# Performance work log

Hardware: AMD Instinct MI355X
Metric: run time of the kernel (lower is better)

## Reference

```python
import jax, jax.numpy as jnp
import numpy as np
from jax import lax

DN = ('NCHW', 'OIHW', 'NCHW')


def _dwconv(x, w, pad_h, pad_w):
    # depthwise conv: feature_group_count == channels
    C = x.shape[1]
    return lax.conv_general_dilated(
        x, w, window_strides=(1, 1),
        padding=[(pad_h, pad_h), (pad_w, pad_w)],
        dimension_numbers=DN, feature_group_count=C)


def setup_inputs() -> dict:
    key = jax.random.key(0)
    ks = jax.random.split(key, 6)
    B, C, H, W = 8, 64, 256, 256
    K = 21
    x = jax.random.normal(ks[0], (B, C, H, W), dtype=jnp.float32)
    local_w = jax.random.normal(ks[1], (C, 1, 5, 5), dtype=jnp.float32) * (2.0 / 25) ** 0.5
    h_w = jax.random.normal(ks[2], (C, 1, 1, K), dtype=jnp.float32) * (2.0 / K) ** 0.5
    v_w = jax.random.normal(ks[3], (C, 1, K, 1), dtype=jnp.float32) * (2.0 / K) ** 0.5
    pw_w = jax.random.normal(ks[4], (C, C, 1, 1), dtype=jnp.float32) * (1.0 / C) ** 0.5
    gamma = jnp.ones((C,), dtype=jnp.float32)
    beta = jnp.zeros((C,), dtype=jnp.float32)
    mean = jnp.zeros((C,), dtype=jnp.float32)
    var = jnp.ones((C,), dtype=jnp.float32)
    return {"x": x, "local_w": local_w, "h_w": h_w, "v_w": v_w,
            "pw_w": pw_w, "gamma": gamma, "beta": beta, "mean": mean, "var": var}


def reference(x, local_w, h_w, v_w, pw_w, gamma, beta, mean, var):
    eps = 1e-5
    attn = _dwconv(x, local_w, 2, 2)        # 5x5 depthwise
    attn = _dwconv(attn, h_w, 0, 10)        # 1x21 depthwise
    attn = _dwconv(attn, v_w, 10, 0)        # 21x1 depthwise
    attn = lax.conv_general_dilated(        # 1x1 pointwise (full mix)
        attn, pw_w, (1, 1), [(0, 0), (0, 0)], dimension_numbers=DN)
    # BatchNorm (inference mode with running stats) fused with sigmoid gate
    inv = gamma * lax.rsqrt(var + eps)
    attn = attn * inv[None, :, None, None] + (beta - mean * inv)[None, :, None, None]
    return x * jax.nn.sigmoid(attn)
```

## Files before the change

kernel.cpp:

```cpp
#include <hip/hip_runtime.h>
#include <hip/hip_bf16.h>

#define BB 8
#define CC 64
#define HH 256
#define WW 256

__device__ __forceinline__ unsigned short f2bf(float f) {
    __hip_bfloat16 h = __float2bfloat16(f);
    return *reinterpret_cast<unsigned short*>(&h);
}
__device__ __forceinline__ float bf2f(unsigned short u) {
    unsigned int v = ((unsigned int)u) << 16;
    float r;
    __builtin_memcpy(&r, &v, 4);
    return r;
}
__device__ __forceinline__ float bflo(unsigned int u) {
    unsigned int v = u << 16;
    float r; __builtin_memcpy(&r, &v, 4); return r;
}
__device__ __forceinline__ float bfhi(unsigned int u) {
    unsigned int v = u & 0xffff0000u;
    float r; __builtin_memcpy(&r, &v, 4); return r;
}

__global__ __launch_bounds__(512) void k1_local_h(
        const float* __restrict__ x, const float* __restrict__ lw,
        const float* __restrict__ hw, unsigned short* __restrict__ a2out) {
    const int strip = blockIdx.x;
    const int bc    = blockIdx.y;
    const int c     = bc & (CC - 1);
    const int y0    = strip * 32;
    const int tid   = threadIdx.x;

    __shared__ float4 xs4[36][66];
    __shared__ float4 a1_4[32][70];

    const float* xbase = x + (size_t)bc * (HH * WW);

    if (tid < 192) {
        int rr = tid / 6, g = tid % 6;
        a1_4[rr][g < 3 ? g : 64 + g] = make_float4(0.f, 0.f, 0.f, 0.f);
    }
    for (int i = tid; i < 36 * 66; i += 512) {
        int rr = i / 66, g = i - rr * 66;
        int gy = y0 - 2 + rr;
        float4 v = make_float4(0.f, 0.f, 0.f, 0.f);
        if (gy >= 0 && gy < HH && g >= 1 && g <= 64)
            v = *reinterpret_cast<const float4*>(xbase + (size_t)gy * WW + 4 * (g - 1));
        xs4[rr][g] = v;
    }
    __syncthreads();

    const int cg = tid & 31;
    const int rp = tid >> 5;
    const float* lwc = lw + c * 25;

    float acc0[8], acc1[8];
    #pragma unroll
    for (int j = 0; j < 8; ++j) { acc0[j] = 0.f; acc1[j] = 0.f; }

    #pragma unroll
    for (int t = 0; t < 6; ++t) {
        float4 g0 = xs4[2 * rp + t][2 * cg + 0];
        float4 g1 = xs4[2 * rp + t][2 * cg + 1];
        float4 g2 = xs4[2 * rp + t][2 * cg + 2];
        float4 g3 = xs4[2 * rp + t][2 * cg + 3];
        float f[16] = {g0.x, g0.y, g0.z, g0.w, g1.x, g1.y, g1.z, g1.w,
                       g2.x, g2.y, g2.z, g2.w, g3.x, g3.y, g3.z, g3.w};
        if (t < 5) {
            #pragma unroll
            for (int kx = 0; kx < 5; ++kx) {
                float wv = lwc[t * 5 + kx];
                #pragma unroll
                for (int j = 0; j < 8; ++j)
                    acc0[j] = fmaf(wv, f[j + kx + 2], acc0[j]);
            }
        }
        if (t >= 1) {
            #pragma unroll
            for (int kx = 0; kx < 5; ++kx) {
                float wv = lwc[(t - 1) * 5 + kx];
                #pragma unroll
                for (int j = 0; j < 8; ++j)
                    acc1[j] = fmaf(wv, f[j + kx + 2], acc1[j]);
            }
        }
    }
    a1_4[2 * rp + 0][2 * cg + 3] = make_float4(acc0[0], acc0[1], acc0[2], acc0[3]);
    a1_4[2 * rp + 0][2 * cg + 4] = make_float4(acc0[4], acc0[5], acc0[6], acc0[7]);
    a1_4[2 * rp + 1][2 * cg + 3] = make_float4(acc1[0], acc1[1], acc1[2], acc1[3]);
    a1_4[2 * rp + 1][2 * cg + 4] = make_float4(acc1[4], acc1[5], acc1[6], acc1[7]);
    __syncthreads();

    const float* hwc = hw + c * 21;
    #pragma unroll
    for (int row = 0; row < 2; ++row) {
        float fw[32];
        #pragma unroll
        for (int t2 = 0; t2 < 8; ++t2) {
            float4 g = a1_4[2 * rp + row][2 * cg + t2];
            fw[4 * t2 + 0] = g.x; fw[4 * t2 + 1] = g.y;
            fw[4 * t2 + 2] = g.z; fw[4 * t2 + 3] = g.w;
        }
        float o[8];
        #pragma unroll
        for (int j = 0; j < 8; ++j) o[j] = 0.f;
        #pragma unroll
        for (int k = 0; k < 21; ++k) {
            float wv = hwc[k];
            #pragma unroll
            for (int j = 0; j < 8; ++j)
                o[j] = fmaf(wv, fw[j + k + 2], o[j]);
        }
        unsigned short* dst = a2out + (size_t)(bc * HH + y0 + 2 * rp + row) * WW + 8 * cg;
        uint4 pk;
        pk.x = (unsigned)f2bf(o[0]) | ((unsigned)f2bf(o[1]) << 16);
        pk.y = (unsigned)f2bf(o[2]) | ((unsigned)f2bf(o[3]) << 16);
        pk.z = (unsigned)f2bf(o[4]) | ((unsigned)f2bf(o[5]) << 16);
        pk.w = (unsigned)f2bf(o[6]) | ((unsigned)f2bf(o[7]) << 16);
        *reinterpret_cast<uint4*>(dst) = pk;
    }
}

__global__ __launch_bounds__(256) void k2a_v(
        const unsigned short* __restrict__ a2, const float* __restrict__ vw,
        unsigned short* __restrict__ a3) {
    const int bx    = blockIdx.x;
    const int strip = bx >> 1;
    const int x0    = (bx & 1) * 128;
    const int bc    = blockIdx.y;
    const int c     = bc & (CC - 1);
    const int y0    = strip * 64;
    const int tid   = threadIdx.x;

    __shared__ unsigned short lds[84][128];

    const unsigned short* sbase = a2 + (size_t)bc * (HH * WW) + x0;
    for (int i = tid; i < 84 * 16; i += 256) {
        int row = i >> 4, g = i & 15;
        int gy = y0 - 10 + row;
        uint4 v = make_uint4(0u, 0u, 0u, 0u);
        if (gy >= 0 && gy < HH)
            v = *reinterpret_cast<const uint4*>(sbase + (size_t)gy * WW + g * 8);
        *reinterpret_cast<uint4*>(&lds[row][g * 8]) = v;
    }
    __syncthreads();

    const float* vwc = vw + c * 21;
    float w[21];
    #pragma unroll
    for (int k = 0; k < 21; ++k) w[k] = vwc[k];

    const int cg = tid & 15;
    const int rg = tid >> 4;
    unsigned short* dst = a3 + (size_t)bc * (HH * WW)
                        + (size_t)(y0 + rg * 4) * WW + x0 + cg * 8;

    #pragma unroll 1
    for (int i = 0; i < 4; ++i) {
        float s0 = 0.f, s1 = 0.f, s2 = 0.f, s3 = 0.f;
        float s4 = 0.f, s5 = 0.f, s6 = 0.f, s7 = 0.f;
        #pragma unroll
        for (int k = 0; k < 21; ++k) {
            uint4 u = *reinterpret_cast<const uint4*>(&lds[rg * 4 + i + k][cg * 8]);
            float wk = w[k];
            s0 = fmaf(wk, bflo(u.x), s0); s1 = fmaf(wk, bfhi(u.x), s1);
            s2 = fmaf(wk, bflo(u.y), s2); s3 = fmaf(wk, bfhi(u.y), s3);
            s4 = fmaf(wk, bflo(u.z), s4); s5 = fmaf(wk, bfhi(u.z), s5);
            s6 = fmaf(wk, bflo(u.w), s6); s7 = fmaf(wk, bfhi(u.w), s7);
        }
        uint4 o;
        o.x = (unsigned int)f2bf(s0) | ((unsigned int)f2bf(s1) << 16);
        o.y = (unsigned int)f2bf(s2) | ((unsigned int)f2bf(s3) << 16);
        o.z = (unsigned int)f2bf(s4) | ((unsigned int)f2bf(s5) << 16);
        o.w = (unsigned int)f2bf(s6) | ((unsigned int)f2bf(s7) << 16);
        *reinterpret_cast<uint4*>(dst + (size_t)i * WW) = o;
    }
}

__global__ __launch_bounds__(512, 4) void k2b_pw(
        const unsigned short* __restrict__ a3, const float* __restrict__ x,
        const float* __restrict__ pw, const float* __restrict__ gamma,
        const float* __restrict__ beta, const float* __restrict__ mean,
        const float* __restrict__ var, float* __restrict__ out) {
    const int y   = blockIdx.x;
    const int b   = blockIdx.y;
    const int tid = threadIdx.x;

    __shared__ unsigned short a3s[64][256];

    const unsigned short* abase = a3 + ((size_t)b * CC * HH + y) * WW;
    for (int i = tid; i < 64 * 64; i += 512) {
        int ci = i >> 6, q = (i & 63) << 2;
        ushort4 v = *reinterpret_cast<const ushort4*>(abase + (size_t)ci * HH * WW + q);
        *reinterpret_cast<ushort4*>(&a3s[ci][q]) = v;
    }
    __syncthreads();

    const int wu = __builtin_amdgcn_readfirstlane(tid >> 6);
    const int l  = tid & 63;

    float acc[32];
    #pragma unroll
    for (int i = 0; i < 32; ++i) acc[i] = 0.f;

    const float* wbase = pw + (size_t)(wu * 8) * 64;

    #pragma unroll
    for (int ch = 0; ch < 16; ++ch) {
        ushort4 q0 = *reinterpret_cast<const ushort4*>(&a3s[4 * ch + 0][l << 2]);
        ushort4 q1 = *reinterpret_cast<const ushort4*>(&a3s[4 * ch + 1][l << 2]);
        ushort4 q2 = *reinterpret_cast<const ushort4*>(&a3s[4 * ch + 2][l << 2]);
        ushort4 q3 = *reinterpret_cast<const ushort4*>(&a3s[4 * ch + 3][l << 2]);
        float p0x = bf2f(q0.x), p0y = bf2f(q0.y), p0z = bf2f(q0.z), p0w = bf2f(q0.w);
        float p1x = bf2f(q1.x), p1y = bf2f(q1.y), p1z = bf2f(q1.z), p1w = bf2f(q1.w);
        float p2x = bf2f(q2.x), p2y = bf2f(q2.y), p2z = bf2f(q2.z), p2w = bf2f(q2.w);
        float p3x = bf2f(q3.x), p3y = bf2f(q3.y), p3z = bf2f(q3.z), p3w = bf2f(q3.w);
        #pragma unroll
        for (int j = 0; j < 8; ++j) {
            float4 w4 = *reinterpret_cast<const float4*>(wbase + (size_t)j * 64 + 4 * ch);
            acc[j * 4 + 0] = fmaf(w4.x, p0x, acc[j * 4 + 0]);
            acc[j * 4 + 0] = fmaf(w4.y, p1x, acc[j * 4 + 0]);
            acc[j * 4 + 0] = fmaf(w4.z, p2x, acc[j * 4 + 0]);
            acc[j * 4 + 0] = fmaf(w4.w, p3x, acc[j * 4 + 0]);
            acc[j * 4 + 1] = fmaf(w4.x, p0y, acc[j * 4 + 1]);
            acc[j * 4 + 1] = fmaf(w4.y, p1y, acc[j * 4 + 1]);
            acc[j * 4 + 1] = fmaf(w4.z, p2y, acc[j * 4 + 1]);
            acc[j * 4 + 1] = fmaf(w4.w, p3y, acc[j * 4 + 1]);
            acc[j * 4 + 2] = fmaf(w4.x, p0z, acc[j * 4 + 2]);
            acc[j * 4 + 2] = fmaf(w4.y, p1z, acc[j * 4 + 2]);
            acc[j * 4 + 2] = fmaf(w4.z, p2z, acc[j * 4 + 2]);
            acc[j * 4 + 2] = fmaf(w4.w, p3z, acc[j * 4 + 2]);
            acc[j * 4 + 3] = fmaf(w4.x, p0w, acc[j * 4 + 3]);
            acc[j * 4 + 3] = fmaf(w4.y, p1w, acc[j * 4 + 3]);
            acc[j * 4 + 3] = fmaf(w4.z, p2w, acc[j * 4 + 3]);
            acc[j * 4 + 3] = fmaf(w4.w, p3w, acc[j * 4 + 3]);
        }
    }

    #pragma unroll
    for (int j = 0; j < 8; ++j) {
        int co = wu * 8 + j;
        float inv = gamma[co] * rsqrtf(var[co] + 1e-5f);
        float sh  = beta[co] - mean[co] * inv;
        size_t off = (((size_t)b * CC + co) * HH + y) * WW + (l << 2);
        float4 xv = *reinterpret_cast<const float4*>(x + off);
        float4 r;
        float a;
        a = acc[j * 4 + 0] * inv + sh; r.x = xv.x / (1.f + __expf(-a));
        a = acc[j * 4 + 1] * inv + sh; r.y = xv.y / (1.f + __expf(-a));
        a = acc[j * 4 + 2] * inv + sh; r.z = xv.z / (1.f + __expf(-a));
        a = acc[j * 4 + 3] * inv + sh; r.w = xv.w / (1.f + __expf(-a));
        *reinterpret_cast<float4*>(out + off) = r;
    }
}

extern "C" void kernel_launch(void* const* d_in, const int* in_sizes, int n_in,
                              void* d_out, int out_size, void* d_ws, size_t ws_size,
                              hipStream_t stream) {
    const float* x     = (const float*)d_in[0];
    const float* lw    = (const float*)d_in[1];
    const float* hw    = (const float*)d_in[2];
    const float* vw    = (const float*)d_in[3];
    const float* pw    = (const float*)d_in[4];
    const float* gamma = (const float*)d_in[5];
    const float* beta  = (const float*)d_in[6];
    const float* mean  = (const float*)d_in[7];
    const float* var   = (const float*)d_in[8];
    float* out = (float*)d_out;

    unsigned short* ws1 = (unsigned short*)d_ws;
    unsigned short* ws2 = ws1 + (size_t)BB * CC * HH * WW;

    k1_local_h<<<dim3(HH / 32, BB * CC), 512, 0, stream>>>(x, lw, hw, ws1);
    k2a_v<<<dim3(8, BB * CC), 256, 0, stream>>>(ws1, vw, ws2);
    k2b_pw<<<dim3(HH, BB), 512, 0, stream>>>(ws2, x, pw, gamma, beta, mean, var, out);
}
```

Baseline: 415.8 us.

## Replace shared-memory staging of 5x5 output with wavefront shuffles for 1x21 conv

The intermediate a1 tile in shared memory is removed, along with its zero-fill and the barrier after it. The 1x21 horizontal depthwise conv now gets its neighbour columns through __shfl_up/__shfl_down across lanes, and zeroes lanes at the row edges. The x tile is stored with even and odd rows split into two halves and a row pitch of 67, which is meant to reduce LDS bank conflicts. The main aim is to roughly halve LDS use per block for higher occupancy. The cost is extra cross-lane shuffle instructions and more register pressure.

Result: slower. 428.1 us (+3.0%).

```diff
diff --git a/kernel.cpp b/kernel.cpp
--- a/kernel.cpp
+++ b/kernel.cpp
@@ -34,22 +34,17 @@
     const int y0    = strip * 32;
     const int tid   = threadIdx.x;
 
-    __shared__ float4 xs4[36][66];
-    __shared__ float4 a1_4[32][70];
+    __shared__ float4 xs4[36][67];
 
     const float* xbase = x + (size_t)bc * (HH * WW);
 
-    if (tid < 192) {
-        int rr = tid / 6, g = tid % 6;
-        a1_4[rr][g < 3 ? g : 64 + g] = make_float4(0.f, 0.f, 0.f, 0.f);
-    }
     for (int i = tid; i < 36 * 66; i += 512) {
         int rr = i / 66, g = i - rr * 66;
         int gy = y0 - 2 + rr;
         float4 v = make_float4(0.f, 0.f, 0.f, 0.f);
         if (gy >= 0 && gy < HH && g >= 1 && g <= 64)
             v = *reinterpret_cast<const float4*>(xbase + (size_t)gy * WW + 4 * (g - 1));
-        xs4[rr][g] = v;
+        xs4[(rr >> 1) + (rr & 1) * 18][g] = v;
     }
     __syncthreads();
 
@@ -63,10 +58,11 @@
 
     #pragma unroll
     for (int t = 0; t < 6; ++t) {
-        float4 g0 = xs4[2 * rp + t][2 * cg + 0];
-        float4 g1 = xs4[2 * rp + t][2 * cg + 1];
-        float4 g2 = xs4[2 * rp + t][2 * cg + 2];
-        float4 g3 = xs4[2 * rp + t][2 * cg + 3];
+        const int pr = 0 + (t >> 1) + (t & 1) * 18;
+        float4 g0 = xs4[rp + pr][2 * cg + 0];
+        float4 g1 = xs4[rp + pr][2 * cg + 1];
+        float4 g2 = xs4[rp + pr][2 * cg + 2];
+        float4 g3 = xs4[rp + pr][2 * cg + 3];
         float f[16] = {g0.x, g0.y, g0.z, g0.w, g1.x, g1.y, g1.z, g1.w,
                        g2.x, g2.y, g2.z, g2.w, g3.x, g3.y, g3.z, g3.w};
         if (t < 5) {
@@ -88,22 +84,37 @@
             }
         }
     }
-    a1_4[2 * rp + 0][2 * cg + 3] = make_float4(acc0[0], acc0[1], acc0[2], acc0[3]);
-    a1_4[2 * rp + 0][2 * cg + 4] = make_float4(acc0[4], acc0[5], acc0[6], acc0[7]);
-    a1_4[2 * rp + 1][2 * cg + 3] = make_float4(acc1[0], acc1[1], acc1[2], acc1[3]);
-    a1_4[2 * rp + 1][2 * cg + 4] = make_float4(acc1[4], acc1[5], acc1[6], acc1[7]);
-    __syncthreads();
 
     const float* hwc = hw + c * 21;
     #pragma unroll
     for (int row = 0; row < 2; ++row) {
-        float fw[32];
-        #pragma unroll
-        for (int t2 = 0; t2 < 8; ++t2) {
-            float4 g = a1_4[2 * rp + row][2 * cg + t2];
-            fw[4 * t2 + 0] = g.x; fw[4 * t2 + 1] = g.y;
-            fw[4 * t2 + 2] = g.z; fw[4 * t2 + 3] = g.w;
-        }
+        float a[8];
+        #pragma unroll
+        for (int j = 0; j < 8; ++j) a[j] = row ? acc1[j] : acc0[j];
+
+        float w28[28];
+        w28[0] = __shfl_up(a[6], 2, 64);
+        w28[1] = __shfl_up(a[7], 2, 64);
+        #pragma unroll
+        for (int j = 0; j < 8; ++j) w28[2 + j]  = __shfl_up(a[j], 1, 64);
+        #pragma unroll
+        for (int j = 0; j < 8; ++j) w28[10 + j] = a[j];
+        #pragma unroll
+        for (int j = 0; j < 8; ++j) w28[18 + j] = __shfl_down(a[j], 1, 64);
+        w28[26] = __shfl_down(a[0], 2, 64);
+        w28[27] = __shfl_down(a[1], 2, 64);
+
+        if (cg < 2)  { w28[0] = 0.f; w28[1] = 0.f; }
+        if (cg < 1)  {
+            #pragma unroll
+            for (int j = 0; j < 8; ++j) w28[2 + j] = 0.f;
+        }
+        if (cg > 30) {
+            #pragma unroll
+            for (int j = 0; j < 8; ++j) w28[18 + j] = 0.f;
+        }
+        if (cg > 29) { w28[26] = 0.f; w28[27] = 0.f; }
+
         float o[8];
         #pragma unroll
         for (int j = 0; j < 8; ++j) o[j] = 0.f;
@@ -112,8 +123,9 @@
             float wv = hwc[k];
             #pragma unroll
             for (int j = 0; j < 8; ++j)
-                o[j] = fmaf(wv, fw[j + k + 2], o[j]);
-        }
+                o[j] = fmaf(wv, w28[j + k], o[j]);
+        }
+
         unsigned short* dst = a2out + (size_t)(bc * HH + y0 + 2 * rp + row) * WW + 8 * cg;
         uint4 pk;
         pk.x = (unsigned)f2bf(o[0]) | ((unsigned)f2bf(o[1]) << 16);
```

## Drop LDS input staging in local+horizontal conv kernel, read x directly per row-pair

Applied to the files above, without the earlier changes.

The fused 5x5 plus 1x21 depthwise kernel no longer stages a 36-row input tile in shared memory. Each 64-thread wave now loops over four row pairs and loads the float4 column and its left and right neighbours straight from global memory. Shared memory is kept only for a small per-wave buffer that holds the horizontal-pass intermediate, and block size drops to 256. The aim is to cut LDS footprint and barrier cost so more blocks fit per CU, at the cost of redundant global/cache reads of overlapping rows and narrower 8-byte bf16 stores.

Measured after the change: 424.1 us. +2.0%, slower.

```diff
diff --git a/kernel.cpp b/kernel.cpp
--- a/kernel.cpp
+++ b/kernel.cpp
@@ -25,7 +25,7 @@
     float r; __builtin_memcpy(&r, &v, 4); return r;
 }
 
-__global__ __launch_bounds__(512) void k1_local_h(
+__global__ __launch_bounds__(256) void k1_local_h(
         const float* __restrict__ x, const float* __restrict__ lw,
         const float* __restrict__ hw, unsigned short* __restrict__ a2out) {
     const int strip = blockIdx.x;
@@ -33,94 +33,88 @@
     const int c     = bc & (CC - 1);
     const int y0    = strip * 32;
     const int tid   = threadIdx.x;
-
-    __shared__ float4 xs4[36][66];
-    __shared__ float4 a1_4[32][70];
-
+    const int cg    = tid & 63;
+    const int rw    = tid >> 6;
+
+    __shared__ float4 arow[4][2][70];
+
+    if (cg < 12) {
+        int rr = cg >= 6 ? 1 : 0;
+        int g6 = cg - 6 * rr;
+        arow[rw][rr][g6 < 3 ? g6 : 64 + g6] = make_float4(0.f, 0.f, 0.f, 0.f);
+    }
+
+    const float* lwc = lw + c * 25;
+    const float* hwc = hw + c * 21;
     const float* xbase = x + (size_t)bc * (HH * WW);
 
-    if (tid < 192) {
-        int rr = tid / 6, g = tid % 6;
-        a1_4[rr][g < 3 ? g : 64 + g] = make_float4(0.f, 0.f, 0.f, 0.f);
-    }
-    for (int i = tid; i < 36 * 66; i += 512) {
-        int rr = i / 66, g = i - rr * 66;
-        int gy = y0 - 2 + rr;
-        float4 v = make_float4(0.f, 0.f, 0.f, 0.f);
-        if (gy >= 0 && gy < HH && g >= 1 && g <= 64)
-            v = *reinterpret_cast<const float4*>(xbase + (size_t)gy * WW + 4 * (g - 1));
-        xs4[rr][g] = v;
-    }
-    __syncthreads();
-
-    const int cg = tid & 31;
-    const int rp = tid >> 5;
-    const float* lwc = lw + c * 25;
-
-    float acc0[8], acc1[8];
-    #pragma unroll
-    for (int j = 0; j < 8; ++j) { acc0[j] = 0.f; acc1[j] = 0.f; }
-
-    #pragma unroll
-    for (int t = 0; t < 6; ++t) {
-        float4 g0 = xs4[2 * rp + t][2 * cg + 0];
-        float4 g1 = xs4[2 * rp + t][2 * cg + 1];
-        float4 g2 = xs4[2 * rp + t][2 * cg + 2];
-        float4 g3 = xs4[2 * rp + t][2 * cg + 3];
-        float f[16] = {g0.x, g0.y, g0.z, g0.w, g1.x, g1.y, g1.z, g1.w,
-                       g2.x, g2.y, g2.z, g2.w, g3.x, g3.y, g3.z, g3.w};
-        if (t < 5) {
+    #pragma unroll 1
+    for (int pr = 0; pr < 4; ++pr) {
+        const int yy = y0 + 8 * rw + 2 * pr;
+        float acc0[4] = {0.f, 0.f, 0.f, 0.f};
+        float acc1[4] = {0.f, 0.f, 0.f, 0.f};
+
+        #pragma unroll
+        for (int t = 0; t < 6; ++t) {
+            const int gy = yy - 2 + t;
+            float4 A = make_float4(0.f, 0.f, 0.f, 0.f);
+            float4 B = A, C = A;
+            if (gy >= 0 && gy < HH) {
+                const float* rp_ = xbase + (size_t)gy * WW + 4 * cg;
+                if (cg > 0)  A = *reinterpret_cast<const float4*>(rp_ - 4);
+                B = *reinterpret_cast<const float4*>(rp_);
+                if (cg < 63) C = *reinterpret_cast<const float4*>(rp_ + 4);
+            }
+            float f[12] = {A.x, A.y, A.z, A.w, B.x, B.y, B.z, B.w,
+                           C.x, C.y, C.z, C.w};
+            if (t < 5) {
+                #pragma unroll
+                for (int kx = 0; kx < 5; ++kx) {
+                    float wv = lwc[t * 5 + kx];
+                    #pragma unroll
+                    for (int j = 0; j < 4; ++j)
+                        acc0[j] = fmaf(wv, f[j + kx + 2], acc0[j]);
+                }
+            }
+            if (t >= 1) {
+                #pragma unroll
+                for (int kx = 0; kx < 5; ++kx) {
+                    float wv = lwc[(t - 1) * 5 + kx];
+                    #pragma unroll
+                    for (int j = 0; j < 4; ++j)
+                        acc1[j] = fmaf(wv, f[j + kx + 2], acc1[j]);
+                }
+            }
+        }
+
+        arow[rw][0][cg + 3] = make_float4(acc0[0], acc0[1], acc0[2], acc0[3]);
+        arow[rw][1][cg + 3] = make_float4(acc1[0], acc1[1], acc1[2], acc1[3]);
+        __syncthreads();
+
+        #pragma unroll
+        for (int row = 0; row < 2; ++row) {
+            float fw[28];
             #pragma unroll
-            for (int kx = 0; kx < 5; ++kx) {
-                float wv = lwc[t * 5 + kx];
+            for (int i2 = 0; i2 < 7; ++i2) {
+                float4 g = arow[rw][row][cg + i2];
+                fw[4 * i2 + 0] = g.x; fw[4 * i2 + 1] = g.y;
+                fw[4 * i2 + 2] = g.z; fw[4 * i2 + 3] = g.w;
+            }
+            float o[4] = {0.f, 0.f, 0.f, 0.f};
+            #pragma unroll
+            for (int k = 0; k < 21; ++k) {
+                float wv = hwc[k];
                 #pragma unroll
-                for (int j = 0; j < 8; ++j)
-                    acc0[j] = fmaf(wv, f[j + kx + 2], acc0[j]);
-            }
-        }
-        if (t >= 1) {
-            #pragma unroll
-            for (int kx = 0; kx < 5; ++kx) {
-                float wv = lwc[(t - 1) * 5 + kx];
-                #pragma unroll
-                for (int j = 0; j < 8; ++j)
-                    acc1[j] = fmaf(wv, f[j + kx + 2], acc1[j]);
-            }
-        }
-    }
-    a1_4[2 * rp + 0][2 * cg + 3] = make_float4(acc0[0], acc0[1], acc0[2], acc0[3]);
-    a1_4[2 * rp + 0][2 * cg + 4] = make_float4(acc0[4], acc0[5], acc0[6], acc0[7]);
-    a1_4[2 * rp + 1][2 * cg + 3] = make_float4(acc1[0], acc1[1], acc1[2], acc1[3]);
-    a1_4[2 * rp + 1][2 * cg + 4] = make_float4(acc1[4], acc1[5], acc1[6], acc1[7]);
-    __syncthreads();
-
-    const float* hwc = hw + c * 21;
-    #pragma unroll
-    for (int row = 0; row < 2; ++row) {
-        float fw[32];
-        #pragma unroll
-        for (int t2 = 0; t2 < 8; ++t2) {
-            float4 g = a1_4[2 * rp + row][2 * cg + t2];
-            fw[4 * t2 + 0] = g.x; fw[4 * t2 + 1] = g.y;
-            fw[4 * t2 + 2] = g.z; fw[4 * t2 + 3] = g.w;
-        }
-        float o[8];
-        #pragma unroll
-        for (int j = 0; j < 8; ++j) o[j] = 0.f;
-        #pragma unroll
-        for (int k = 0; k < 21; ++k) {
-            float wv = hwc[k];
-            #pragma unroll
-            for (int j = 0; j < 8; ++j)
-                o[j] = fmaf(wv, fw[j + k + 2], o[j]);
-        }
-        unsigned short* dst = a2out + (size_t)(bc * HH + y0 + 2 * rp + row) * WW + 8 * cg;
-        uint4 pk;
-        pk.x = (unsigned)f2bf(o[0]) | ((unsigned)f2bf(o[1]) << 16);
-        pk.y = (unsigned)f2bf(o[2]) | ((unsigned)f2bf(o[3]) << 16);
-        pk.z = (unsigned)f2bf(o[4]) | ((unsigned)f2bf(o[5]) << 16);
-        pk.w = (unsigned)f2bf(o[6]) | ((unsigned)f2bf(o[7]) << 16);
-        *reinterpret_cast<uint4*>(dst) = pk;
+                for (int j = 0; j < 4; ++j)
+                    o[j] = fmaf(wv, fw[j + k + 2], o[j]);
+            }
+            unsigned short* dst =
+                a2out + (size_t)(bc * HH + yy + row) * WW + 4 * cg;
+            ushort4 pk;
+            pk.x = f2bf(o[0]); pk.y = f2bf(o[1]);
+            pk.z = f2bf(o[2]); pk.w = f2bf(o[3]);
+            *reinterpret_cast<ushort4*>(dst) = pk;
+        }
     }
 }
 
@@ -274,7 +268,7 @@
     unsigned short* ws1 = (unsigned short*)d_ws;
     unsigned short* ws2 = ws1 + (size_t)BB * CC * HH * WW;
 
-    k1_local_h<<<dim3(HH / 32, BB * CC), 512, 0, stream>>>(x, lw, hw, ws1);
+    k1_local_h<<<dim3(HH / 32, BB * CC), 256, 0, stream>>>(x, lw, hw, ws1);
     k2a_v<<<dim3(8, BB * CC), 256, 0, stream>>>(ws1, vw, ws2);
     k2b_pw<<<dim3(HH, BB), 512, 0, stream>>>(ws2, x, pw, gamma, beta, mean, var, out);
 }
```
